# Performance work log

Hardware: AMD Instinct MI355X
Metric: run time of the kernel (lower is better)

## Reference

```python
import jax, jax.numpy as jnp
import numpy as np

B, S, D, H = 8, 1500, 1024, 16
HD = D // H
DFF = 4 * D
EPS = 1e-5


def _xavier(key, shape):
    fan_in, fan_out = shape[1], shape[0]
    limit = float(np.sqrt(6.0 / (fan_in + fan_out)))
    return jax.random.uniform(key, shape, jnp.float32, -limit, limit)


def setup_inputs() -> dict:
    key = jax.random.key(0)
    ks = jax.random.split(key, 8)
    return {
        "hidden_states": jax.random.normal(ks[0], (B, S, D), jnp.float32),
        "Wq": _xavier(ks[1], (D, D)),
        "Wk": _xavier(ks[2], (D, D)),
        "Wv": _xavier(ks[3], (D, D)),
        "Wo": _xavier(ks[4], (D, D)),
        "W1": _xavier(ks[5], (DFF, D)),
        "b1": jnp.zeros((DFF,), jnp.float32),
        "W2": _xavier(ks[6], (D, DFF)),
        "b2": jnp.zeros((D,), jnp.float32),
        "ln1_g": jnp.ones((D,), jnp.float32),
        "ln1_b": jnp.zeros((D,), jnp.float32),
        "ln2_g": jnp.ones((D,), jnp.float32),
        "ln2_b": jnp.zeros((D,), jnp.float32),
    }


def _layernorm(x, g, b):
    mu = jnp.mean(x, axis=-1, keepdims=True)
    var = jnp.mean(jnp.square(x - mu), axis=-1, keepdims=True)
    return (x - mu) * jax.lax.rsqrt(var + EPS) * g + b


def reference(hidden_states, Wq, Wk, Wv, Wo, W1, b1, W2, b2, ln1_g, ln1_b, ln2_g, ln2_b):
    x = hidden_states
    residual = x
    h = _layernorm(x, ln1_g, ln1_b)
    # torch Linear: y = h @ W.T ; reshape to heads
    q = (h @ Wq.T).reshape(B, S, H, HD).transpose(0, 2, 1, 3) * (HD ** -0.5)
    k = (h @ Wk.T).reshape(B, S, H, HD).transpose(0, 2, 1, 3)
    v = (h @ Wv.T).reshape(B, S, H, HD).transpose(0, 2, 1, 3)
    scores = jnp.einsum('bhqd,bhkd->bhqk', q, k)
    attn = jax.nn.softmax(scores.astype(jnp.float32), axis=-1).astype(h.dtype)
    ctx = jnp.einsum('bhqk,bhkd->bhqd', attn, v)
    ctx = ctx.transpose(0, 2, 1, 3).reshape(B, S, D)
    x = residual + ctx @ Wo.T
    residual = x
    h = _layernorm(x, ln2_g, ln2_b)
    ffn = jax.nn.gelu(h @ W1.T + b1, approximate=False) @ W2.T + b2
    return residual + ffn
```

## Files before the change

kernel.cpp:

```cpp
#include <hip/hip_runtime.h>
#include <hip/hip_bf16.h>
#include <cstdint>
#include <cstddef>

#define B_    8
#define S_    1500
#define D_    1024
#define H_    16
#define HD_   64
#define DFF_  4096
#define M_    12000
#define VTS_  1536

typedef __bf16 bf16;
typedef __attribute__((ext_vector_type(8))) __bf16 bf16x8;
typedef __attribute__((ext_vector_type(4))) float f32x4;

#define MFMA16(a, b, c) __builtin_amdgcn_mfma_f32_16x16x32_bf16((a), (b), (c), 0, 0, 0)

static __device__ __forceinline__ void gload16(const void* g, void* l) {
  __builtin_amdgcn_global_load_lds(
      (const __attribute__((address_space(1))) void*)(uintptr_t)g,
      (__attribute__((address_space(3))) void*)(uintptr_t)l, 16, 0, 0);
}

static __device__ __forceinline__ unsigned short f2bu(float v) {
  bf16 h = (bf16)v;
  union { bf16 h; unsigned short u; } c;
  c.h = h;
  return c.u;
}

static constexpr size_t HSZ      = (size_t)M_ * D_ * 2;
static constexpr size_t H_OFF    = 0;
static constexpr size_t WQ_OFF   = H_OFF + HSZ;
static constexpr size_t WK_OFF   = WQ_OFF + (size_t)D_ * D_ * 2;
static constexpr size_t WV_OFF   = WK_OFF + (size_t)D_ * D_ * 2;
static constexpr size_t WO_OFF   = WV_OFF + (size_t)D_ * D_ * 2;
static constexpr size_t Q_OFF    = WO_OFF + (size_t)D_ * D_ * 2;
static constexpr size_t K_OFF    = Q_OFF + HSZ;
static constexpr size_t VT_OFF   = K_OFF + HSZ;
static constexpr size_t W1_OFF   = VT_OFF + (size_t)128 * 64 * VTS_ * 2;
static constexpr size_t W2_OFF   = W1_OFF + (size_t)DFF_ * D_ * 2;
static constexpr size_t WS_BASE  = W2_OFF + (size_t)DFF_ * D_ * 2;
static constexpr size_t H2B_OFF  = WS_BASE;
static constexpr size_t NEED_BIG = WS_BASE + HSZ;
static constexpr size_t H2F_OFF  = VT_OFF;
static constexpr size_t ACT_OFF  = 0;

__launch_bounds__(256)
__global__ void cvt_bf16(const float* __restrict__ src, bf16* __restrict__ dst, int n) {
  int i = (blockIdx.x * 256 + threadIdx.x) * 4;
  if (i < n) {
    float4 f = *(const float4*)(src + i);
    dst[i + 0] = (bf16)f.x;
    dst[i + 1] = (bf16)f.y;
    dst[i + 2] = (bf16)f.z;
    dst[i + 3] = (bf16)f.w;
  }
}

__launch_bounds__(256)
__global__ void ln_fused(const float* __restrict__ x, const float* __restrict__ g,
                         const float* __restrict__ bb, bf16* __restrict__ out) {
  const int row = blockIdx.x;
  const int t = threadIdx.x;
  const float4 xv = *(const float4*)(x + (size_t)row * D_ + t * 4);
  float s  = xv.x + xv.y + xv.z + xv.w;
  float s2 = xv.x * xv.x + xv.y * xv.y + xv.z * xv.z + xv.w * xv.w;
#pragma unroll
  for (int m = 32; m >= 1; m >>= 1) {
    s  += __shfl_xor(s, m);
    s2 += __shfl_xor(s2, m);
  }
  __shared__ float red[8];
  const int w = t >> 6;
  if ((t & 63) == 0) { red[w] = s; red[4 + w] = s2; }
  __syncthreads();
  s  = red[0] + red[1] + red[2] + red[3];
  s2 = red[4] + red[5] + red[6] + red[7];
  const float mu  = s * (1.0f / D_);
  const float var = s2 * (1.0f / D_) - mu * mu;
  const float rs  = rsqrtf(var + 1e-5f);
  const float4 gv = *(const float4*)(g + t * 4);
  const float4 bv = *(const float4*)(bb + t * 4);
  bf16* o = out + (size_t)row * D_ + t * 4;
  o[0] = (bf16)((xv.x - mu) * rs * gv.x + bv.x);
  o[1] = (bf16)((xv.y - mu) * rs * gv.y + bv.y);
  o[2] = (bf16)((xv.z - mu) * rs * gv.z + bv.z);
  o[3] = (bf16)((xv.w - mu) * rs * gv.w + bv.w);
}

template <int EPI>
__launch_bounds__(1024, 4)
__global__ void gemm256(const bf16* __restrict__ A, const bf16* __restrict__ Bw,
                        int M, int N, int K, int nbx, int nby,
                        bf16* __restrict__ outB, float* outF,
                        const float* __restrict__ bias, const float* resid,
                        bf16* __restrict__ outQ, bf16* __restrict__ outK2,
                        bf16* __restrict__ outV) {
  __shared__ bf16 a_lds[2][256 * 64];
  __shared__ bf16 b_lds[2][256 * 64];

  const int nwg = nbx * nby;
  const int lid = blockIdx.x;
  const int xcd = lid & 7;
  const int q8 = nwg >> 3, r8 = nwg & 7;
  const int wgid = (xcd < r8 ? xcd * (q8 + 1) : r8 * (q8 + 1) + (xcd - r8) * q8) + (lid >> 3);
  const int bx = wgid / nby;
  const int by = wgid - bx * nby;

  const int t = threadIdx.x;
  const int lane = t & 63, wid = t >> 6;
  const int wm = wid >> 2, wn = wid & 3;
  const int l15 = lane & 15, hi = lane >> 4;
  const int l7 = l15 & 7;
  const int mrow0 = bx * 256;
  const int ncol0 = by * 256;

  const int rl = t >> 3;
  const int sc8 = ((t & 7) ^ (rl & 7)) << 3;
  unsigned offA[2], offB[2];
#pragma unroll
  for (int j = 0; j < 2; ++j) {
    int gr = mrow0 + j * 128 + rl; gr = gr < M ? gr : M - 1;
    offA[j] = (unsigned)gr * (unsigned)K + (unsigned)sc8;
    offB[j] = (unsigned)(ncol0 + j * 128 + rl) * (unsigned)K + (unsigned)sc8;
  }

  f32x4 acc[4][4] = {};

  const int NT = K >> 6;

  {
    char* ad = (char*)&a_lds[0][0];
    char* bd = (char*)&b_lds[0][0];
    gload16(A + offA[0], ad + t * 16);
    gload16(A + offA[1], ad + 16384 + t * 16);
    gload16(Bw + offB[0], bd + t * 16);
    gload16(Bw + offB[1], bd + 16384 + t * 16);
  }
  __syncthreads();

  int buf = 0;
  for (int tt = 0; tt < NT; ++tt) {
    if (tt + 1 < NT) {
      const unsigned k1 = (unsigned)(tt + 1) << 6;
      char* ad = (char*)&a_lds[buf ^ 1][0];
      char* bd = (char*)&b_lds[buf ^ 1][0];
      gload16(A + offA[0] + k1, ad + t * 16);
      gload16(A + offA[1] + k1, ad + 16384 + t * 16);
      gload16(Bw + offB[0] + k1, bd + t * 16);
      gload16(Bw + offB[1] + k1, bd + 16384 + t * 16);
    }

    const bf16* al = &a_lds[buf][0];
    const bf16* bl = &b_lds[buf][0];
#pragma unroll
    for (int kk = 0; kk < 2; ++kk) {
      bf16x8 af_[4], bf_[4];
      const int cc = ((kk * 4 + hi) ^ l7) << 3;
#pragma unroll
      for (int m = 0; m < 4; ++m)
        af_[m] = *(const bf16x8*)&al[(wm * 64 + m * 16 + l15) * 64 + cc];
#pragma unroll
      for (int n = 0; n < 4; ++n)
        bf_[n] = *(const bf16x8*)&bl[(wn * 64 + n * 16 + l15) * 64 + cc];
      __builtin_amdgcn_s_setprio(1);
#pragma unroll
      for (int m = 0; m < 4; ++m)
#pragma unroll
        for (int n = 0; n < 4; ++n)
          acc[m][n] = MFMA16(af_[m], bf_[n], acc[m][n]);
      __builtin_amdgcn_s_setprio(0);
    }

    __syncthreads();
    buf ^= 1;
  }

  const int r0 = hi * 4;

  if constexpr (EPI == 5) {
    const int mm = by >> 2;
    const int nloc0 = (by & 3) * 256;
    if (mm == 2) {
#pragma unroll
      for (int m = 0; m < 4; ++m) {
        int row0 = mrow0 + wm * 64 + m * 16 + r0;
        if (row0 < M) {
          int bb2 = row0 / 1500;
          int s = row0 - bb2 * 1500;
#pragma unroll
          for (int n = 0; n < 4; ++n) {
            int f = nloc0 + wn * 64 + n * 16 + l15;
            size_t a = ((size_t)(bb2 * 16 + (f >> 6)) * 64 + (f & 63)) * VTS_ + s;
            ushort4 pk;
            pk.x = f2bu(acc[m][n][0]);
            pk.y = f2bu(acc[m][n][1]);
            pk.z = f2bu(acc[m][n][2]);
            pk.w = f2bu(acc[m][n][3]);
            *reinterpret_cast<ushort4*>((unsigned short*)outV + a) = pk;
          }
        }
      }
    } else {
      bf16* dst = (mm == 0) ? outQ : outK2;
      const float sc = (mm == 0) ? 0.18033688011112042f : 1.0f;
#pragma unroll
      for (int m = 0; m < 4; ++m) {
#pragma unroll
        for (int n = 0; n < 4; ++n) {
          int col = nloc0 + wn * 64 + n * 16 + l15;
#pragma unroll
          for (int r = 0; r < 4; ++r) {
            int row = mrow0 + wm * 64 + m * 16 + r0 + r;
            if (row < M) dst[(size_t)row * D_ + col] = (bf16)(acc[m][n][r] * sc);
          }
        }
      }
    }
    return;
  }

#pragma unroll
  for (int m = 0; m < 4; ++m) {
#pragma unroll
    for (int n = 0; n < 4; ++n) {
      int col = ncol0 + wn * 64 + n * 16 + l15;
#pragma unroll
      for (int r = 0; r < 4; ++r) {
        int row = mrow0 + wm * 64 + m * 16 + r0 + r;
        if (row < M) {
          float v = acc[m][n][r];
          if constexpr (EPI == 2) {
            float xg = v + bias[col];
            v = 0.5f * xg * (1.0f + erff(xg * 0.70710678118654752f));
            outB[(size_t)row * N + col] = (bf16)v;
          }
          if constexpr (EPI == 3) {
            v += resid[(size_t)row * N + col];
            if (bias) v += bias[col];
            outF[(size_t)row * N + col] = v;
          }
        }
      }
    }
  }
}

template <int EPI>
__launch_bounds__(256)
__global__ void gemm_bt(const bf16* __restrict__ A, const bf16* __restrict__ Bw,
                        int M, int N, int K,
                        bf16* __restrict__ outB, float* outF,
                        const float* __restrict__ bias, const float* resid,
                        float scale) {
  __shared__ bf16 a_lds[128 * 64];
  __shared__ bf16 b_lds[128 * 64];
  const int t = threadIdx.x;
  const int lane = t & 63, wid = t >> 6;
  const int wr = wid >> 1, wc = wid & 1;
  const int mrow0 = blockIdx.x * 128;
  const int ncol0 = blockIdx.y * 128;
  const int l15 = lane & 15;
  const int khi = (lane >> 4) << 3;

  f32x4 acc[4][4] = {};

  for (int k0 = 0; k0 < K; k0 += 64) {
#pragma unroll
    for (int i = 0; i < 4; ++i) {
      int idx = i * 2048 + t * 8;
      int row = idx >> 6, col = idx & 63;
      int gr = mrow0 + row;
      gr = gr < M ? gr : M - 1;
      gload16(A + (size_t)gr * K + (k0 + col), (char*)a_lds + idx * 2);
    }
#pragma unroll
    for (int i = 0; i < 4; ++i) {
      int idx = i * 2048 + t * 8;
      int row = idx >> 6, col = idx & 63;
      gload16(Bw + (size_t)(ncol0 + row) * K + (k0 + col), (char*)b_lds + idx * 2);
    }
    __syncthreads();
#pragma unroll
    for (int kk = 0; kk < 2; ++kk) {
      bf16x8 af[4], bfv[4];
#pragma unroll
      for (int m = 0; m < 4; ++m)
        af[m] = *(const bf16x8*)&a_lds[(wr * 64 + m * 16 + l15) * 64 + kk * 32 + khi];
#pragma unroll
      for (int n = 0; n < 4; ++n)
        bfv[n] = *(const bf16x8*)&b_lds[(wc * 64 + n * 16 + l15) * 64 + kk * 32 + khi];
#pragma unroll
      for (int m = 0; m < 4; ++m)
#pragma unroll
        for (int n = 0; n < 4; ++n)
          acc[m][n] = MFMA16(af[m], bfv[n], acc[m][n]);
    }
    __syncthreads();
  }

  const int r0 = (lane >> 4) << 2;
#pragma unroll
  for (int m = 0; m < 4; ++m) {
#pragma unroll
    for (int n = 0; n < 4; ++n) {
      int col = ncol0 + wc * 64 + n * 16 + l15;
#pragma unroll
      for (int r = 0; r < 4; ++r) {
        int row = mrow0 + wr * 64 + m * 16 + r0 + r;
        if (row < M) {
          float v = acc[m][n][r];
          if constexpr (EPI == 2) {
            float xg = v + bias[col];
            v = 0.5f * xg * (1.0f + erff(xg * 0.70710678118654752f));
          }
          if constexpr (EPI == 3) {
            v += resid[(size_t)row * N + col];
            if (bias) v += bias[col];
            outF[(size_t)row * N + col] = v;
          } else {
            outB[(size_t)row * N + col] = (bf16)v;
          }
        }
      }
    }
  }
}

__launch_bounds__(256, 4)
__global__ void attn_fwd6(const bf16* __restrict__ q, const bf16* __restrict__ kg,
                          const bf16* __restrict__ vt, bf16* __restrict__ cx) {
  __shared__ bf16 k_lds[2][64 * 64];
  __shared__ bf16 v_lds[2][64 * 64];
  __shared__ bf16 p_lds[4][16 * 64];

  const int t = threadIdx.x;
  const int lane = t & 63, w = t >> 6;
  const int L = blockIdx.x;
  const int wu = (L & 7) * 384 + (L >> 3);
  const int bh = wu / 24;
  const int qt = wu - bh * 24;
  const int l15 = lane & 15;
  const int hi = lane >> 4;
  const int khi = hi << 3;

  const size_t hoff = ((size_t)(bh >> 4) * S_) * D_ + (size_t)(bh & 15) * HD_;
  const bf16* qh = q + hoff;
  const bf16* kh = kg + hoff;
  const bf16* vh = vt + (size_t)bh * (64 * VTS_);

  const int st_r0 = t >> 3;
  const int st_c  = t & 7;

  int qr = qt * 64 + w * 16 + l15;
  int qrc = qr < S_ ? qr : S_ - 1;
  const bf16x8 qf0 = *(const bf16x8*)(qh + (size_t)qrc * D_ + khi);
  const bf16x8 qf1 = *(const bf16x8*)(qh + (size_t)qrc * D_ + 32 + khi);

  f32x4 oacc[4] = {};
  float mrun[4], lrun[4];
#pragma unroll
  for (int r = 0; r < 4; ++r) { mrun[r] = -1e30f; lrun[r] = 0.f; }

  bf16* pw = &p_lds[w][0];
  const int NT = (S_ + 63) / 64;
  const float THR = 11.5415605f;

#pragma unroll
  for (int i = 0; i < 2; ++i) {
    int row = i * 32 + st_r0;
    int sc = st_c ^ (row & 7);
    int key = row < S_ ? row : S_ - 1;
    gload16(kh + (size_t)key * D_ + sc * 8, (char*)&k_lds[0][0] + (i * 2048 + t * 8) * 2);
    gload16(vh + (size_t)row * VTS_ + sc * 8, (char*)&v_lds[0][0] + (i * 2048 + t * 8) * 2);
  }
  __syncthreads();

  int buf = 0;
  for (int kt = 0; kt < NT; ++kt) {
    if (kt + 1 < NT) {
      int kb = (kt + 1) * 64;
#pragma unroll
      for (int i = 0; i < 2; ++i) {
        int row = i * 32 + st_r0;
        int sc = st_c ^ (row & 7);
        int key = kb + row;
        key = key < S_ ? key : S_ - 1;
        gload16(kh + (size_t)key * D_ + sc * 8,
                (char*)&k_lds[buf ^ 1][0] + (i * 2048 + t * 8) * 2);
        gload16(vh + (size_t)row * VTS_ + kb + sc * 8,
                (char*)&v_lds[buf ^ 1][0] + (i * 2048 + t * 8) * 2);
      }
    }

    float pv[4][4];
    __builtin_amdgcn_s_setprio(1);
#pragma unroll
    for (int nb = 0; nb < 4; ++nb) {
      int krow = nb * 16 + l15;
      f32x4 z = {};
      z = MFMA16(qf0, *(const bf16x8*)&k_lds[buf][krow * 64 + ((hi ^ (l15 & 7)) << 3)], z);
      z = MFMA16(qf1, *(const bf16x8*)&k_lds[buf][krow * 64 + (((4 + hi) ^ (l15 & 7)) << 3)], z);
#pragma unroll
      for (int r = 0; r < 4; ++r) pv[nb][r] = z[r];
    }
    __builtin_amdgcn_s_setprio(0);

    if (kt == NT - 1) {
#pragma unroll
      for (int nb = 0; nb < 4; ++nb) {
        bool cvld = (kt * 64 + nb * 16 + l15) < S_;
#pragma unroll
        for (int r = 0; r < 4; ++r) pv[nb][r] = cvld ? pv[nb][r] : -1e30f;
      }
    }

    float lmax[4];
    bool ok = true;
#pragma unroll
    for (int r = 0; r < 4; ++r) {
      lmax[r] = fmaxf(fmaxf(pv[0][r], pv[1][r]), fmaxf(pv[2][r], pv[3][r]));
      ok = ok && (lmax[r] <= mrun[r] + THR);
    }
    if (!__all(ok)) {
#pragma unroll
      for (int r = 0; r < 4; ++r) {
        float mx = lmax[r];
        mx = fmaxf(mx, __shfl_xor(mx, 1));
        mx = fmaxf(mx, __shfl_xor(mx, 2));
        mx = fmaxf(mx, __shfl_xor(mx, 4));
        mx = fmaxf(mx, __shfl_xor(mx, 8));
        float mnew = fmaxf(mrun[r], mx);
        float corr = exp2f(mrun[r] - mnew);
        lrun[r] *= corr;
        mrun[r] = mnew;
#pragma unroll
        for (int db = 0; db < 4; ++db) oacc[db][r] *= corr;
      }
    }

#pragma unroll
    for (int r = 0; r < 4; ++r) {
      float p0 = exp2f(pv[0][r] - mrun[r]);
      float p1 = exp2f(pv[1][r] - mrun[r]);
      float p2 = exp2f(pv[2][r] - mrun[r]);
      float p3 = exp2f(pv[3][r] - mrun[r]);
      pv[0][r] = p0; pv[1][r] = p1; pv[2][r] = p2; pv[3][r] = p3;
      lrun[r] += (p0 + p1) + (p2 + p3);
    }

#pragma unroll
    for (int nb = 0; nb < 4; ++nb) {
#pragma unroll
      for (int r = 0; r < 4; ++r) {
        int prow = hi * 4 + r;
        int pcol = (nb * 16 + l15) ^ ((prow & 7) << 3);
        pw[prow * 64 + pcol] = (bf16)pv[nb][r];
      }
    }

    __builtin_amdgcn_s_setprio(1);
#pragma unroll
    for (int kk = 0; kk < 2; ++kk) {
      bf16x8 pf = *(const bf16x8*)&pw[l15 * 64 + (((kk * 4 + hi) ^ (l15 & 7)) << 3)];
#pragma unroll
      for (int db = 0; db < 4; ++db) {
        int vrow = db * 16 + l15;
        bf16x8 vf = *(const bf16x8*)&v_lds[buf][vrow * 64 + (((kk * 4 + hi) ^ (l15 & 7)) << 3)];
        oacc[db] = MFMA16(pf, vf, oacc[db]);
      }
    }
    __builtin_amdgcn_s_setprio(0);

    __syncthreads();
    buf ^= 1;
  }

#pragma unroll
  for (int r = 0; r < 4; ++r) {
    float ps = lrun[r];
    ps += __shfl_xor(ps, 1);
    ps += __shfl_xor(ps, 2);
    ps += __shfl_xor(ps, 4);
    ps += __shfl_xor(ps, 8);
    int qrow = qt * 64 + w * 16 + hi * 4 + r;
    if (qrow < S_) {
      float inv = 1.0f / ps;
#pragma unroll
      for (int db = 0; db < 4; ++db)
        cx[hoff + (size_t)qrow * D_ + db * 16 + l15] = (bf16)(oacc[db][r] * inv);
    }
  }
}

extern "C" void kernel_launch(void* const* d_in, const int* in_sizes, int n_in,
                              void* d_out, int out_size, void* d_ws, size_t ws_size,
                              hipStream_t stream) {
  const float* x   = (const float*)d_in[0];
  const float* Wq  = (const float*)d_in[1];
  const float* Wk  = (const float*)d_in[2];
  const float* Wv  = (const float*)d_in[3];
  const float* Wo  = (const float*)d_in[4];
  const float* W1  = (const float*)d_in[5];
  const float* b1  = (const float*)d_in[6];
  const float* W2  = (const float*)d_in[7];
  const float* b2  = (const float*)d_in[8];
  const float* g1  = (const float*)d_in[9];
  const float* be1 = (const float*)d_in[10];
  const float* g2  = (const float*)d_in[11];
  const float* be2 = (const float*)d_in[12];
  float* out = (float*)d_out;

  char* ws = (char*)d_ws;
  bf16* h_b   = (bf16*)(ws + H_OFF);
  bf16* wq_b  = (bf16*)(ws + WQ_OFF);
  bf16* wk_b  = (bf16*)(ws + WK_OFF);
  bf16* wv_b  = (bf16*)(ws + WV_OFF);
  bf16* wo_b  = (bf16*)(ws + WO_OFF);
  bf16* w1_b  = (bf16*)(ws + W1_OFF);
  bf16* w2_b  = (bf16*)(ws + W2_OFF);
  bf16* q_b   = (bf16*)(ws + Q_OFF);
  bf16* k_b   = (bf16*)(ws + K_OFF);
  bf16* vt_b  = (bf16*)(ws + VT_OFF);
  bf16* act_b = (bf16*)(ws + ACT_OFF);
  bf16* ctx_b = h_b;

  const bool big = ws_size >= NEED_BIG;
  bf16* h2_b = (bf16*)(ws + (big ? H2B_OFF : H2F_OFF));

  cvt_bf16<<<(D_ * D_) / 1024, 256, 0, stream>>>(Wq, wq_b, D_ * D_);
  cvt_bf16<<<(D_ * D_) / 1024, 256, 0, stream>>>(Wk, wk_b, D_ * D_);
  cvt_bf16<<<(D_ * D_) / 1024, 256, 0, stream>>>(Wv, wv_b, D_ * D_);
  cvt_bf16<<<(D_ * D_) / 1024, 256, 0, stream>>>(Wo, wo_b, D_ * D_);
  cvt_bf16<<<(DFF_ * D_) / 1024, 256, 0, stream>>>(W1, w1_b, DFF_ * D_);
  cvt_bf16<<<(DFF_ * D_) / 1024, 256, 0, stream>>>(W2, w2_b, DFF_ * D_);

  ln_fused<<<M_, 256, 0, stream>>>(x, g1, be1, h_b);

  gemm256<5><<<47 * 12, 1024, 0, stream>>>(
      h_b, wq_b, M_, 3072, D_, 47, 12, nullptr, nullptr, nullptr, nullptr, q_b, k_b, vt_b);

  attn_fwd6<<<3072, 256, 0, stream>>>(q_b, k_b, vt_b, ctx_b);

  gemm256<3><<<47 * 4, 1024, 0, stream>>>(
      ctx_b, wo_b, M_, D_, D_, 47, 4, nullptr, out, nullptr, x, nullptr, nullptr, nullptr);

  ln_fused<<<M_, 256, 0, stream>>>(out, g2, be2, h2_b);

  if (big) {
    gemm256<2><<<47 * 16, 1024, 0, stream>>>(
        h2_b, w1_b, M_, DFF_, D_, 47, 16, act_b, nullptr, b1, nullptr,
        nullptr, nullptr, nullptr);
    gemm256<3><<<47 * 4, 1024, 0, stream>>>(
        act_b, w2_b, M_, D_, DFF_, 47, 4, nullptr, out, b2, out,
        nullptr, nullptr, nullptr);
  } else {
    for (int c = 0; c < 3; ++c) {
      int r0c = c * 4000;
      int nr = 4000;
      int mt = (nr + 255) / 256;
      gemm256<2><<<mt * 16, 1024, 0, stream>>>(
          h2_b + (size_t)r0c * D_, w1_b, nr, DFF_, D_, mt, 16, act_b, nullptr, b1, nullptr,
          nullptr, nullptr, nullptr);
      gemm_bt<3><<<dim3((nr + 127) / 128, D_ / 128), 256, 0, stream>>>(
          act_b, w2_b, nr, D_, DFF_, nullptr, out + (size_t)r0c * D_, b2,
          out + (size_t)r0c * D_, 0.f);
    }
  }
}
```

Baseline: 643.0 us.

## Single-buffer attention K/V tiles with split loads to raise occupancy

The attention kernel drops double-buffered K and V tiles in LDS for single buffers. It now loads the next K tile right after QK^T and the next V tile after PV, so each tile's load overlaps the other half of the iteration. Launch bounds rise from 4 to 6 blocks per SM to use the smaller LDS footprint for more resident waves. The cost is an extra barrier per iteration and less prefetch distance, and the higher occupancy target may force register spills.

```diff
diff --git a/kernel.cpp b/kernel.cpp
--- a/kernel.cpp
+++ b/kernel.cpp
@@ -330,11 +330,11 @@
   }
 }
 
-__launch_bounds__(256, 4)
-__global__ void attn_fwd6(const bf16* __restrict__ q, const bf16* __restrict__ kg,
+__launch_bounds__(256, 6)
+__global__ void attn_fwd8(const bf16* __restrict__ q, const bf16* __restrict__ kg,
                           const bf16* __restrict__ vt, bf16* __restrict__ cx) {
-  __shared__ bf16 k_lds[2][64 * 64];
-  __shared__ bf16 v_lds[2][64 * 64];
+  __shared__ bf16 k_lds[64 * 64];
+  __shared__ bf16 v_lds[64 * 64];
   __shared__ bf16 p_lds[4][16 * 64];
 
   const int t = threadIdx.x;
@@ -374,13 +374,28 @@
     int row = i * 32 + st_r0;
     int sc = st_c ^ (row & 7);
     int key = row < S_ ? row : S_ - 1;
-    gload16(kh + (size_t)key * D_ + sc * 8, (char*)&k_lds[0][0] + (i * 2048 + t * 8) * 2);
-    gload16(vh + (size_t)row * VTS_ + sc * 8, (char*)&v_lds[0][0] + (i * 2048 + t * 8) * 2);
-  }
-  __syncthreads();
-
-  int buf = 0;
+    gload16(kh + (size_t)key * D_ + sc * 8, (char*)&k_lds[0] + (i * 2048 + t * 8) * 2);
+    gload16(vh + (size_t)row * VTS_ + sc * 8, (char*)&v_lds[0] + (i * 2048 + t * 8) * 2);
+  }
+
   for (int kt = 0; kt < NT; ++kt) {
+    __syncthreads();
+
+    float pv[4][4];
+    __builtin_amdgcn_s_setprio(1);
+#pragma unroll
+    for (int nb = 0; nb < 4; ++nb) {
+      int krow = nb * 16 + l15;
+      f32x4 z = {};
+      z = MFMA16(qf0, *(const bf16x8*)&k_lds[krow * 64 + ((hi ^ (l15 & 7)) << 3)], z);
+      z = MFMA16(qf1, *(const bf16x8*)&k_lds[krow * 64 + (((4 + hi) ^ (l15 & 7)) << 3)], z);
+#pragma unroll
+      for (int r = 0; r < 4; ++r) pv[nb][r] = z[r];
+    }
+    __builtin_amdgcn_s_setprio(0);
+
+    __syncthreads();
+
     if (kt + 1 < NT) {
       int kb = (kt + 1) * 64;
 #pragma unroll
@@ -390,24 +405,9 @@
         int key = kb + row;
         key = key < S_ ? key : S_ - 1;
         gload16(kh + (size_t)key * D_ + sc * 8,
-                (char*)&k_lds[buf ^ 1][0] + (i * 2048 + t * 8) * 2);
-        gload16(vh + (size_t)row * VTS_ + kb + sc * 8,
-                (char*)&v_lds[buf ^ 1][0] + (i * 2048 + t * 8) * 2);
-      }
-    }
-
-    float pv[4][4];
-    __builtin_amdgcn_s_setprio(1);
-#pragma unroll
-    for (int nb = 0; nb < 4; ++nb) {
-      int krow = nb * 16 + l15;
-      f32x4 z = {};
-      z = MFMA16(qf0, *(const bf16x8*)&k_lds[buf][krow * 64 + ((hi ^ (l15 & 7)) << 3)], z);
-      z = MFMA16(qf1, *(const bf16x8*)&k_lds[buf][krow * 64 + (((4 + hi) ^ (l15 & 7)) << 3)], z);
-#pragma unroll
-      for (int r = 0; r < 4; ++r) pv[nb][r] = z[r];
-    }
-    __builtin_amdgcn_s_setprio(0);
+                (char*)&k_lds[0] + (i * 2048 + t * 8) * 2);
+      }
+    }
 
     if (kt == NT - 1) {
 #pragma unroll
@@ -469,14 +469,24 @@
 #pragma unroll
       for (int db = 0; db < 4; ++db) {
         int vrow = db * 16 + l15;
-        bf16x8 vf = *(const bf16x8*)&v_lds[buf][vrow * 64 + (((kk * 4 + hi) ^ (l15 & 7)) << 3)];
+        bf16x8 vf = *(const bf16x8*)&v_lds[vrow * 64 + (((kk * 4 + hi) ^ (l15 & 7)) << 3)];
         oacc[db] = MFMA16(pf, vf, oacc[db]);
       }
     }
     __builtin_amdgcn_s_setprio(0);
 
     __syncthreads();
-    buf ^= 1;
+
+    if (kt + 1 < NT) {
+      int kb = (kt + 1) * 64;
+#pragma unroll
+      for (int i = 0; i < 2; ++i) {
+        int row = i * 32 + st_r0;
+        int sc = st_c ^ (row & 7);
+        gload16(vh + (size_t)row * VTS_ + kb + sc * 8,
+                (char*)&v_lds[0] + (i * 2048 + t * 8) * 2);
+      }
+    }
   }
 
 #pragma unroll
@@ -543,7 +553,7 @@
   gemm256<5><<<47 * 12, 1024, 0, stream>>>(
       h_b, wq_b, M_, 3072, D_, 47, 12, nullptr, nullptr, nullptr, nullptr, q_b, k_b, vt_b);
 
-  attn_fwd6<<<3072, 256, 0, stream>>>(q_b, k_b, vt_b, ctx_b);
+  attn_fwd8<<<3072, 256, 0, stream>>>(q_b, k_b, vt_b, ctx_b);
 
   gemm256<3><<<47 * 4, 1024, 0, stream>>>(
       ctx_b, wo_b, M_, D_, D_, 47, 4, nullptr, out, nullptr, x, nullptr, nullptr, nullptr);
```

New measurement: 656.8 us. 1.02x slower.
